# Kernel optimization log

Measured on AMD Instinct MI355X. Metric: run time of the kernel, lower is better.

The kernel has to match this reference:

```python
import jax, jax.numpy as jnp
import numpy as np

B, NB, H, C = 32, 1024, 768, 64


def setup_inputs() -> dict:
    key = jax.random.key(0)
    k1, k2, k3, k4, k5, k6 = jax.random.split(key, 6)
    block_tokens = jax.random.normal(k1, (B, NB, H), dtype=jnp.float32)
    block_active = jax.random.randint(k2, (B, NB), 0, 2) == 1
    block_to_channel_map = jax.random.randint(k3, (NB,), 0, C, dtype=jnp.int64)
    # agg_gate params: Linear(H, H//2) -> Tanh -> Linear(H//2, 1)
    s1 = 1.0 / np.sqrt(H)
    s2 = 1.0 / np.sqrt(H // 2)
    W1 = jax.random.uniform(k4, (H, H // 2), jnp.float32, -s1, s1)
    b1 = jnp.zeros((H // 2,), jnp.float32)
    W2 = jax.random.uniform(k5, (H // 2, 1), jnp.float32, -s2, s2)
    b2 = jnp.zeros((1,), jnp.float32)
    return {"block_tokens": block_tokens, "block_active": block_active,
            "block_to_channel_map": block_to_channel_map,
            "W1": W1, "b1": b1, "W2": W2, "b2": b2}


def reference(block_tokens, block_active, block_to_channel_map, W1, b1, W2, b2):
    # gate MLP: (B, NB)
    h = jnp.tanh(jnp.einsum('bnh,hk->bnk', block_tokens, W1) + b1)
    gate = (jnp.einsum('bnk,ko->bno', h, W2) + b2).squeeze(-1)  # (B, NB)

    # (C, NB) one-hot channel membership; (B, C, NB) active-per-channel mask
    onehot = block_to_channel_map[None, :] == jnp.arange(C)[:, None]
    mask = block_active[:, None, :] & onehot[None, :, :]  # (B, C, NB)

    neg_inf = jnp.float32(-jnp.inf)
    g = jnp.where(mask, gate[:, None, :], neg_inf)  # (B, C, NB)
    m = jnp.max(g, axis=-1, keepdims=True)
    m_safe = jnp.where(jnp.isfinite(m), m, 0.0)  # guard all-masked channels
    e = jnp.where(mask, jnp.exp(g - m_safe), 0.0)
    s = jnp.sum(e, axis=-1, keepdims=True)
    w = jnp.where(s > 0, e / jnp.where(s > 0, s, 1.0), 0.0)  # softmax, nan->0

    channel_tokens = jnp.einsum('bcn,bnh->bch', w, block_tokens)  # (B, C, H)
    channel_active = jnp.any(mask, axis=-1)  # (B, C)
    return channel_tokens, channel_active
```

## Files before the change

### kernel.cpp

```cpp
#include <hip/hip_runtime.h>
#include <math.h>

#define B_    32
#define NB_   1024
#define H_    768
#define K_    384
#define C_    64
#define ROWS_ 128
#define NSTEP_ 24

typedef __attribute__((ext_vector_type(8))) short bf16x8;
typedef __attribute__((ext_vector_type(4))) float f32x4;

__device__ __forceinline__ short f2bf(float f) {
    unsigned u = __float_as_uint(f);
    unsigned r = (u + 0x7fffu + ((u >> 16) & 1u)) >> 16;
    return (short)r;
}
__device__ __forceinline__ float ftanh(float x) {
    float e = __expf(2.f * x);
    return 1.f - 2.f * __builtin_amdgcn_rcpf(e + 1.f);
}

__global__ __launch_bounds__(256) void prep_w1(const float* __restrict__ W1,
                                               short* __restrict__ swz)
{
    int idx = blockIdx.x * 256 + threadIdx.x;
    int k = idx / K_, n = idx % K_;
    float v = W1[idx];
    int s = k >> 5, g = (k >> 3) & 3, i = k & 7;
    int t = n >> 4, nn = n & 15;
    swz[((s * 24 + t) * 512) + (g * 16 + nn) * 8 + i] = f2bf(v);
}

__global__ __launch_bounds__(1024) void compact_kernel(
    const int* __restrict__ active, int* __restrict__ list, int* __restrict__ cnt)
{
    __shared__ int wsum[16];
    __shared__ int wbase[17];
    const int b = blockIdx.x, tid = threadIdx.x, lane = tid & 63, wid = tid >> 6;
    const int flag = active[b * NB_ + tid] != 0;
    const unsigned long long m = __ballot(flag);
    if (lane == 0) wsum[wid] = __popcll(m);
    __syncthreads();
    if (tid == 0) {
        int r = 0;
        for (int i = 0; i < 16; ++i) { wbase[i] = r; r += wsum[i]; }
        wbase[16] = r;
        cnt[b] = r;
    }
    __syncthreads();
    const int total = wbase[16];
    if (flag) {
        const int pos = wbase[wid] + __popcll(m & ((1ull << lane) - 1ull));
        list[b * NB_ + pos] = tid;
    }
    if (tid >= total) list[b * NB_ + tid] = 0;
}

__global__ __launch_bounds__(512) void gate_kernel(
    const float* __restrict__ tokens, const short* __restrict__ swz,
    const float* __restrict__ b1, const float* __restrict__ W2,
    const float* __restrict__ b2, const int* __restrict__ list,
    const int* __restrict__ cnt, float* __restrict__ gate)
{
    __shared__ __align__(16) short As[2][4096];
    __shared__ float red[8][128];

    const int b = blockIdx.x >> 3;
    const int chunk = blockIdx.x & 7;
    if (chunk * ROWS_ >= cnt[b]) return;

    const int tid = threadIdx.x;
    const int lane = tid & 63;
    const int w = tid >> 6;

    const int arow = tid >> 2;
    const int akc  = tid & 3;
    const int nrow = list[b * NB_ + chunk * ROWS_ + arow];
    const float* aptr = tokens + ((size_t)b * NB_ + nrow) * H_ + akc * 8;

    const int aoff = (arow >> 4) * 512 + (((akc * 16 + (arow & 15)) ^ (akc * 2)) * 8);
    const int roff = (lane ^ ((lane >> 4) * 2)) * 8;
    const short* bbase = swz + (w * 3) * 512 + lane * 8;

    f32x4 acc[3][8];
#pragma unroll
    for (int j = 0; j < 3; ++j)
#pragma unroll
        for (int f = 0; f < 8; ++f) acc[j][f] = (f32x4){0.f, 0.f, 0.f, 0.f};

    float4 pe0 = *(const float4*)(aptr);
    float4 pe1 = *(const float4*)(aptr + 4);
    float4 po0 = *(const float4*)(aptr + 32);
    float4 po1 = *(const float4*)(aptr + 36);
    bf16x8 be0 = *(const bf16x8*)(bbase);
    bf16x8 be1 = *(const bf16x8*)(bbase + 512);
    bf16x8 be2 = *(const bf16x8*)(bbase + 1024);
    bf16x8 bo0 = be0, bo1 = be1, bo2 = be2;
    {
        bf16x8 av = {f2bf(pe0.x), f2bf(pe0.y), f2bf(pe0.z), f2bf(pe0.w),
                     f2bf(pe1.x), f2bf(pe1.y), f2bf(pe1.z), f2bf(pe1.w)};
        *(bf16x8*)&As[0][aoff] = av;
    }
    asm volatile("s_waitcnt lgkmcnt(0)" ::: "memory");
    __builtin_amdgcn_s_barrier();
    __builtin_amdgcn_sched_barrier(0);

#define GATE_ITER(S, PA0, PA1, QA0, QA1, BC0, BC1, BC2, BN0, BN1, BN2)        \
    do {                                                                      \
        if ((S) + 2 < NSTEP_) {                                               \
            PA0 = *(const float4*)(aptr + ((S) + 2) * 32);                    \
            PA1 = *(const float4*)(aptr + ((S) + 2) * 32 + 4);                \
        }                                                                     \
        if ((S) + 1 < NSTEP_) {                                               \
            const short* bp = bbase + ((S) + 1) * 12288;                      \
            BN0 = *(const bf16x8*)(bp);                                       \
            BN1 = *(const bf16x8*)(bp + 512);                                 \
            BN2 = *(const bf16x8*)(bp + 1024);                                \
            bf16x8 av = {f2bf(QA0.x), f2bf(QA0.y), f2bf(QA0.z), f2bf(QA0.w),  \
                         f2bf(QA1.x), f2bf(QA1.y), f2bf(QA1.z), f2bf(QA1.w)}; \
            *(bf16x8*)&As[((S) + 1) & 1][aoff] = av;                          \
        }                                                                     \
        _Pragma("unroll")                                                     \
        for (int f = 0; f < 8; ++f) {                                         \
            bf16x8 af = *(const bf16x8*)&As[(S) & 1][f * 512 + roff];         \
            acc[0][f] = __builtin_amdgcn_mfma_f32_16x16x32_bf16(af, BC0, acc[0][f], 0, 0, 0); \
            acc[1][f] = __builtin_amdgcn_mfma_f32_16x16x32_bf16(af, BC1, acc[1][f], 0, 0, 0); \
            acc[2][f] = __builtin_amdgcn_mfma_f32_16x16x32_bf16(af, BC2, acc[2][f], 0, 0, 0); \
        }                                                                     \
        asm volatile("s_waitcnt lgkmcnt(0)" ::: "memory");                    \
        __builtin_amdgcn_s_barrier();                                         \
        __builtin_amdgcn_sched_barrier(0);                                    \
    } while (0)

    for (int s = 0; s < NSTEP_; s += 2) {
        GATE_ITER(s,     pe0, pe1, po0, po1, be0, be1, be2, bo0, bo1, bo2);
        GATE_ITER(s + 1, po0, po1, pe0, pe1, bo0, bo1, bo2, be0, be1, be2);
    }
#undef GATE_ITER

    float ps[8][4];
#pragma unroll
    for (int f = 0; f < 8; ++f)
#pragma unroll
        for (int r = 0; r < 4; ++r) ps[f][r] = 0.f;

#pragma unroll
    for (int j = 0; j < 3; ++j) {
        const int n = (w * 3 + j) * 16 + (lane & 15);
        const float bb = b1[n];
        const float ww = W2[n];
#pragma unroll
        for (int f = 0; f < 8; ++f)
#pragma unroll
            for (int r = 0; r < 4; ++r)
                ps[f][r] += ftanh(acc[j][f][r] + bb) * ww;
    }
#pragma unroll
    for (int m = 1; m < 16; m <<= 1)
#pragma unroll
        for (int f = 0; f < 8; ++f)
#pragma unroll
            for (int r = 0; r < 4; ++r)
                ps[f][r] += __shfl_xor(ps[f][r], m, 64);

    if ((lane & 15) == 0) {
        const int rbase = (lane >> 4) * 4;
#pragma unroll
        for (int f = 0; f < 8; ++f)
#pragma unroll
            for (int r = 0; r < 4; ++r)
                red[w][f * 16 + rbase + r] = ps[f][r];
    }
    __syncthreads();
    if (tid < ROWS_) {
        float sg = b2[0];
#pragma unroll
        for (int q = 0; q < 8; ++q) sg += red[q][tid];
        gate[b * NB_ + list[b * NB_ + chunk * ROWS_ + tid]] = sg;
    }
}

__global__ __launch_bounds__(256) void agg_kernel(
    const float* __restrict__ tokens, const int* __restrict__ active,
    const int* __restrict__ cmap, const float* __restrict__ gate,
    float* __restrict__ out_tok, float* __restrict__ out_act)
{
    __shared__ float wls[NB_];
    __shared__ float red[256];
    __shared__ int   idxs[NB_];
    __shared__ float wts[NB_];
    __shared__ int   gbase[17];

    const int b = blockIdx.x >> 6, c = blockIdx.x & 63;
    const int tid = threadIdx.x, lane = tid & 63, wid = tid >> 6;

    float lmax = -INFINITY;
    for (int n = tid; n < NB_; n += 256) {
        const bool msk = (active[b * NB_ + n] != 0) && (cmap[n] == c);
        const float g  = msk ? gate[b * NB_ + n] : -INFINITY;
        wls[n] = g;
        lmax = fmaxf(lmax, g);
    }
    red[tid] = lmax; __syncthreads();
    for (int s = 128; s > 0; s >>= 1) {
        if (tid < s) red[tid] = fmaxf(red[tid], red[tid + s]);
        __syncthreads();
    }
    const float m = red[0]; __syncthreads();
    const float msafe = (m > -INFINITY) ? m : 0.f;

    float lsum = 0.f;
    for (int n = tid; n < NB_; n += 256) {
        const float g = wls[n];
        const float e = (g > -INFINITY) ? __expf(g - msafe) : 0.f;
        wls[n] = e; lsum += e;
    }
    red[tid] = lsum; __syncthreads();
    for (int s = 128; s > 0; s >>= 1) {
        if (tid < s) red[tid] += red[tid + s];
        __syncthreads();
    }
    const float ssum = red[0];
    const float inv  = (ssum > 0.f) ? 1.f / ssum : 0.f;
    __syncthreads();

#pragma unroll
    for (int it = 0; it < 4; ++it) {
        const int n = it * 256 + wid * 64 + lane;
        const unsigned long long mask = __ballot(wls[n] > 0.f);
        if (lane == 0) gbase[1 + it * 4 + wid] = __popcll(mask);
    }
    __syncthreads();
    if (tid == 0) {
        gbase[0] = 0;
        for (int i = 1; i <= 16; ++i) gbase[i] += gbase[i - 1];
    }
    __syncthreads();
#pragma unroll
    for (int it = 0; it < 4; ++it) {
        const int n = it * 256 + wid * 64 + lane;
        const float e = wls[n];
        const unsigned long long mask = __ballot(e > 0.f);
        if (e > 0.f) {
            const int pos = gbase[it * 4 + wid] +
                            __popcll(mask & ((1ull << lane) - 1ull));
            idxs[pos] = n;
            wts[pos]  = e * inv;
        }
    }
    __syncthreads();
    const int cnt = gbase[16];

    float a0 = 0.f, a1 = 0.f, a2 = 0.f;
    const float* tb = tokens + (size_t)b * NB_ * H_;
    for (int i = 0; i < cnt; ++i) {
        const float wv = wts[i];
        const float* t = tb + (size_t)idxs[i] * H_;
        a0 += wv * t[tid];
        a1 += wv * t[tid + 256];
        a2 += wv * t[tid + 512];
    }
    float* o = out_tok + ((size_t)(b * C_ + c)) * H_;
    o[tid]       = a0;
    o[tid + 256] = a1;
    o[tid + 512] = a2;
    if (tid == 0) out_act[b * C_ + c] = (m > -INFINITY) ? 1.f : 0.f;
}

extern "C" void kernel_launch(void* const* d_in, const int* in_sizes, int n_in,
                              void* d_out, int out_size, void* d_ws, size_t ws_size,
                              hipStream_t stream)
{
    const float* tokens = (const float*)d_in[0];
    const int*   active = (const int*)  d_in[1];
    const int*   cmap   = (const int*)  d_in[2];
    const float* W1     = (const float*)d_in[3];
    const float* b1     = (const float*)d_in[4];
    const float* W2     = (const float*)d_in[5];
    const float* b2     = (const float*)d_in[6];

    float* out      = (float*)d_out;
    float* out_act  = out + (size_t)B_ * C_ * H_;

    short* swz     = (short*)d_ws;
    float* gate_ws = (float*)((char*)d_ws + 589824);
    int*   list    = (int*)  ((char*)d_ws + 720896);
    int*   cntb    = (int*)  ((char*)d_ws + 851968);

    compact_kernel<<<B_, 1024, 0, stream>>>(active, list, cntb);
    prep_w1<<<(H_ * K_) / 256, 256, 0, stream>>>(W1, swz);
    gate_kernel<<<B_ * 8, 512, 0, stream>>>(tokens, swz, b1, W2, b2, list, cntb, gate_ws);
    agg_kernel<<<B_ * C_, 256, 0, stream>>>(tokens, active, cmap, gate_ws, out, out_act);
}
```

Before: 55.94 us.

## Shrink gate tiles to 32 rows with 256-thread blocks; vectorize agg loads

The gate GEMM now uses 32-row tiles and 256-thread blocks, giving 1024 blocks instead of 256. Each wave covers 6 N-tiles over 2 row fragments, and occupancy is hinted at 3 blocks per SM. This spreads the active rows over more CUs, at the cost of reloading the W1 slices once per block, which means more global traffic for B. The aggregation kernel switches to float4 loads using 192 threads, cutting the instruction count but leaving a quarter of the threads idle.

```diff
diff --git a/kernel.cpp b/kernel.cpp
--- a/kernel.cpp
+++ b/kernel.cpp
@@ -6,7 +6,7 @@
 #define H_    768
 #define K_    384
 #define C_    64
-#define ROWS_ 128
+#define ROWS_ 32
 #define NSTEP_ 24
 
 typedef __attribute__((ext_vector_type(8))) short bf16x8;
@@ -58,126 +58,158 @@
     if (tid >= total) list[b * NB_ + tid] = 0;
 }
 
-__global__ __launch_bounds__(512) void gate_kernel(
+__global__ __launch_bounds__(256, 3) void gate_kernel(
     const float* __restrict__ tokens, const short* __restrict__ swz,
     const float* __restrict__ b1, const float* __restrict__ W2,
     const float* __restrict__ b2, const int* __restrict__ list,
     const int* __restrict__ cnt, float* __restrict__ gate)
 {
-    __shared__ __align__(16) short As[2][4096];
-    __shared__ float red[8][128];
-
-    const int b = blockIdx.x >> 3;
-    const int chunk = blockIdx.x & 7;
+    __shared__ __align__(16) short As[2][1024];
+    __shared__ float red[4][32];
+
+    const int b = blockIdx.x >> 5;
+    const int chunk = blockIdx.x & 31;
     if (chunk * ROWS_ >= cnt[b]) return;
 
     const int tid = threadIdx.x;
     const int lane = tid & 63;
     const int w = tid >> 6;
 
-    const int arow = tid >> 2;
-    const int akc  = tid & 3;
-    const int nrow = list[b * NB_ + chunk * ROWS_ + arow];
-    const float* aptr = tokens + ((size_t)b * NB_ + nrow) * H_ + akc * 8;
-
-    const int aoff = (arow >> 4) * 512 + (((akc * 16 + (arow & 15)) ^ (akc * 2)) * 8);
-    const int roff = (lane ^ ((lane >> 4) * 2)) * 8;
-    const short* bbase = swz + (w * 3) * 512 + lane * 8;
-
-    f32x4 acc[3][8];
-#pragma unroll
-    for (int j = 0; j < 3; ++j)
-#pragma unroll
-        for (int f = 0; f < 8; ++f) acc[j][f] = (f32x4){0.f, 0.f, 0.f, 0.f};
-
-    float4 pe0 = *(const float4*)(aptr);
-    float4 pe1 = *(const float4*)(aptr + 4);
-    float4 po0 = *(const float4*)(aptr + 32);
-    float4 po1 = *(const float4*)(aptr + 36);
+    const int r   = tid >> 3;
+    const int c8  = tid & 7;
+    const int g2w = c8 >> 1, hw = c8 & 1;
+    const int fw  = r >> 4,  roww = r & 15;
+    const int woff = ((fw * 4 + g2w) * 16 + (roww ^ (g2w << 1))) * 8 + hw * 4;
+    const int nrow = list[b * NB_ + chunk * ROWS_ + r];
+    const float* aptr = tokens + ((size_t)b * NB_ + nrow) * H_ + c8 * 4;
+
+    const int g2r  = lane >> 4;
+    const int rowr = (lane & 15) ^ (g2r << 1);
+    const int roff0 = ((0 + g2r) * 16 + rowr) * 8;
+    const int roff1 = ((4 + g2r) * 16 + rowr) * 8;
+
+    const short* bbase = swz + (w * 6) * 512 + lane * 8;
+
+    f32x4 acc[6][2];
+#pragma unroll
+    for (int j = 0; j < 6; ++j)
+#pragma unroll
+        for (int f = 0; f < 2; ++f) acc[j][f] = (f32x4){0.f, 0.f, 0.f, 0.f};
+
+    float4 pe = *(const float4*)(aptr);
+    float4 po = *(const float4*)(aptr + 32);
     bf16x8 be0 = *(const bf16x8*)(bbase);
     bf16x8 be1 = *(const bf16x8*)(bbase + 512);
     bf16x8 be2 = *(const bf16x8*)(bbase + 1024);
-    bf16x8 bo0 = be0, bo1 = be1, bo2 = be2;
+    bf16x8 be3 = *(const bf16x8*)(bbase + 1536);
+    bf16x8 be4 = *(const bf16x8*)(bbase + 2048);
+    bf16x8 be5 = *(const bf16x8*)(bbase + 2560);
+    bf16x8 bo0 = be0, bo1 = be1, bo2 = be2, bo3 = be3, bo4 = be4, bo5 = be5;
     {
-        bf16x8 av = {f2bf(pe0.x), f2bf(pe0.y), f2bf(pe0.z), f2bf(pe0.w),
-                     f2bf(pe1.x), f2bf(pe1.y), f2bf(pe1.z), f2bf(pe1.w)};
-        *(bf16x8*)&As[0][aoff] = av;
+        short4 av = {f2bf(pe.x), f2bf(pe.y), f2bf(pe.z), f2bf(pe.w)};
+        *(short4*)&As[0][woff] = av;
     }
     asm volatile("s_waitcnt lgkmcnt(0)" ::: "memory");
     __builtin_amdgcn_s_barrier();
     __builtin_amdgcn_sched_barrier(0);
 
-#define GATE_ITER(S, PA0, PA1, QA0, QA1, BC0, BC1, BC2, BN0, BN1, BN2)        \
+#define MFMA_STEP(BUF, B0, B1, B2, B3, B4, B5)                                \
     do {                                                                      \
-        if ((S) + 2 < NSTEP_) {                                               \
-            PA0 = *(const float4*)(aptr + ((S) + 2) * 32);                    \
-            PA1 = *(const float4*)(aptr + ((S) + 2) * 32 + 4);                \
-        }                                                                     \
-        if ((S) + 1 < NSTEP_) {                                               \
-            const short* bp = bbase + ((S) + 1) * 12288;                      \
-            BN0 = *(const bf16x8*)(bp);                                       \
-            BN1 = *(const bf16x8*)(bp + 512);                                 \
-            BN2 = *(const bf16x8*)(bp + 1024);                                \
-            bf16x8 av = {f2bf(QA0.x), f2bf(QA0.y), f2bf(QA0.z), f2bf(QA0.w),  \
-                         f2bf(QA1.x), f2bf(QA1.y), f2bf(QA1.z), f2bf(QA1.w)}; \
-            *(bf16x8*)&As[((S) + 1) & 1][aoff] = av;                          \
-        }                                                                     \
-        _Pragma("unroll")                                                     \
-        for (int f = 0; f < 8; ++f) {                                         \
-            bf16x8 af = *(const bf16x8*)&As[(S) & 1][f * 512 + roff];         \
-            acc[0][f] = __builtin_amdgcn_mfma_f32_16x16x32_bf16(af, BC0, acc[0][f], 0, 0, 0); \
-            acc[1][f] = __builtin_amdgcn_mfma_f32_16x16x32_bf16(af, BC1, acc[1][f], 0, 0, 0); \
-            acc[2][f] = __builtin_amdgcn_mfma_f32_16x16x32_bf16(af, BC2, acc[2][f], 0, 0, 0); \
-        }                                                                     \
-        asm volatile("s_waitcnt lgkmcnt(0)" ::: "memory");                    \
-        __builtin_amdgcn_s_barrier();                                         \
-        __builtin_amdgcn_sched_barrier(0);                                    \
+        bf16x8 a0 = *(const bf16x8*)&As[BUF][roff0];                          \
+        bf16x8 a1 = *(const bf16x8*)&As[BUF][roff1];                          \
+        acc[0][0] = __builtin_amdgcn_mfma_f32_16x16x32_bf16(a0, B0, acc[0][0], 0, 0, 0); \
+        acc[0][1] = __builtin_amdgcn_mfma_f32_16x16x32_bf16(a1, B0, acc[0][1], 0, 0, 0); \
+        acc[1][0] = __builtin_amdgcn_mfma_f32_16x16x32_bf16(a0, B1, acc[1][0], 0, 0, 0); \
+        acc[1][1] = __builtin_amdgcn_mfma_f32_16x16x32_bf16(a1, B1, acc[1][1], 0, 0, 0); \
+        acc[2][0] = __builtin_amdgcn_mfma_f32_16x16x32_bf16(a0, B2, acc[2][0], 0, 0, 0); \
+        acc[2][1] = __builtin_amdgcn_mfma_f32_16x16x32_bf16(a1, B2, acc[2][1], 0, 0, 0); \
+        acc[3][0] = __builtin_amdgcn_mfma_f32_16x16x32_bf16(a0, B3, acc[3][0], 0, 0, 0); \
+        acc[3][1] = __builtin_amdgcn_mfma_f32_16x16x32_bf16(a1, B3, acc[3][1], 0, 0, 0); \
+        acc[4][0] = __builtin_amdgcn_mfma_f32_16x16x32_bf16(a0, B4, acc[4][0], 0, 0, 0); \
+        acc[4][1] = __builtin_amdgcn_mfma_f32_16x16x32_bf16(a1, B4, acc[4][1], 0, 0, 0); \
+        acc[5][0] = __builtin_amdgcn_mfma_f32_16x16x32_bf16(a0, B5, acc[5][0], 0, 0, 0); \
+        acc[5][1] = __builtin_amdgcn_mfma_f32_16x16x32_bf16(a1, B5, acc[5][1], 0, 0, 0); \
     } while (0)
 
     for (int s = 0; s < NSTEP_; s += 2) {
-        GATE_ITER(s,     pe0, pe1, po0, po1, be0, be1, be2, bo0, bo1, bo2);
-        GATE_ITER(s + 1, po0, po1, pe0, pe1, bo0, bo1, bo2, be0, be1, be2);
-    }
-#undef GATE_ITER
-
-    float ps[8][4];
-#pragma unroll
-    for (int f = 0; f < 8; ++f)
-#pragma unroll
-        for (int r = 0; r < 4; ++r) ps[f][r] = 0.f;
-
-#pragma unroll
-    for (int j = 0; j < 3; ++j) {
-        const int n = (w * 3 + j) * 16 + (lane & 15);
+        if (s + 2 < NSTEP_) pe = *(const float4*)(aptr + (s + 2) * 32);
+        if (s + 1 < NSTEP_) {
+            const short* bp = bbase + (s + 1) * 12288;
+            bo0 = *(const bf16x8*)(bp);
+            bo1 = *(const bf16x8*)(bp + 512);
+            bo2 = *(const bf16x8*)(bp + 1024);
+            bo3 = *(const bf16x8*)(bp + 1536);
+            bo4 = *(const bf16x8*)(bp + 2048);
+            bo5 = *(const bf16x8*)(bp + 2560);
+        }
+        MFMA_STEP(0, be0, be1, be2, be3, be4, be5);
+        if (s + 1 < NSTEP_) {
+            short4 av = {f2bf(po.x), f2bf(po.y), f2bf(po.z), f2bf(po.w)};
+            *(short4*)&As[1][woff] = av;
+        }
+        asm volatile("s_waitcnt lgkmcnt(0)" ::: "memory");
+        __builtin_amdgcn_s_barrier();
+        __builtin_amdgcn_sched_barrier(0);
+
+        if (s + 3 < NSTEP_) po = *(const float4*)(aptr + (s + 3) * 32);
+        if (s + 2 < NSTEP_) {
+            const short* bp = bbase + (s + 2) * 12288;
+            be0 = *(const bf16x8*)(bp);
+            be1 = *(const bf16x8*)(bp + 512);
+            be2 = *(const bf16x8*)(bp + 1024);
+            be3 = *(const bf16x8*)(bp + 1536);
+            be4 = *(const bf16x8*)(bp + 2048);
+            be5 = *(const bf16x8*)(bp + 2560);
+        }
+        MFMA_STEP(1, bo0, bo1, bo2, bo3, bo4, bo5);
+        if (s + 2 < NSTEP_) {
+            short4 av = {f2bf(pe.x), f2bf(pe.y), f2bf(pe.z), f2bf(pe.w)};
+            *(short4*)&As[0][woff] = av;
+        }
+        asm volatile("s_waitcnt lgkmcnt(0)" ::: "memory");
+        __builtin_amdgcn_s_barrier();
+        __builtin_amdgcn_sched_barrier(0);
+    }
+#undef MFMA_STEP
+
+    float ps[2][4];
+#pragma unroll
+    for (int f = 0; f < 2; ++f)
+#pragma unroll
+        for (int rr = 0; rr < 4; ++rr) ps[f][rr] = 0.f;
+
+#pragma unroll
+    for (int j = 0; j < 6; ++j) {
+        const int n = (w * 6 + j) * 16 + (lane & 15);
         const float bb = b1[n];
         const float ww = W2[n];
 #pragma unroll
-        for (int f = 0; f < 8; ++f)
-#pragma unroll
-            for (int r = 0; r < 4; ++r)
-                ps[f][r] += ftanh(acc[j][f][r] + bb) * ww;
+        for (int f = 0; f < 2; ++f)
+#pragma unroll
+            for (int rr = 0; rr < 4; ++rr)
+                ps[f][rr] += ftanh(acc[j][f][rr] + bb) * ww;
     }
 #pragma unroll
     for (int m = 1; m < 16; m <<= 1)
 #pragma unroll
-        for (int f = 0; f < 8; ++f)
-#pragma unroll
-            for (int r = 0; r < 4; ++r)
-                ps[f][r] += __shfl_xor(ps[f][r], m, 64);
+        for (int f = 0; f < 2; ++f)
+#pragma unroll
+            for (int rr = 0; rr < 4; ++rr)
+                ps[f][rr] += __shfl_xor(ps[f][rr], m, 64);
 
     if ((lane & 15) == 0) {
         const int rbase = (lane >> 4) * 4;
 #pragma unroll
-        for (int f = 0; f < 8; ++f)
-#pragma unroll
-            for (int r = 0; r < 4; ++r)
-                red[w][f * 16 + rbase + r] = ps[f][r];
+        for (int f = 0; f < 2; ++f)
+#pragma unroll
+            for (int rr = 0; rr < 4; ++rr)
+                red[w][f * 16 + rbase + rr] = ps[f][rr];
     }
     __syncthreads();
     if (tid < ROWS_) {
         float sg = b2[0];
 #pragma unroll
-        for (int q = 0; q < 8; ++q) sg += red[q][tid];
+        for (int q = 0; q < 4; ++q) sg += red[q][tid];
         gate[b * NB_ + list[b * NB_ + chunk * ROWS_ + tid]] = sg;
     }
 }
@@ -253,19 +285,18 @@
     __syncthreads();
     const int cnt = gbase[16];
 
-    float a0 = 0.f, a1 = 0.f, a2 = 0.f;
-    const float* tb = tokens + (size_t)b * NB_ * H_;
-    for (int i = 0; i < cnt; ++i) {
-        const float wv = wts[i];
-        const float* t = tb + (size_t)idxs[i] * H_;
-        a0 += wv * t[tid];
-        a1 += wv * t[tid + 256];
-        a2 += wv * t[tid + 512];
-    }
-    float* o = out_tok + ((size_t)(b * C_ + c)) * H_;
-    o[tid]       = a0;
-    o[tid + 256] = a1;
-    o[tid + 512] = a2;
+    if (tid < 192) {
+        const int d = tid * 4;
+        const float* tb = tokens + (size_t)b * NB_ * H_ + d;
+        float4 a = {0.f, 0.f, 0.f, 0.f};
+        for (int i = 0; i < cnt; ++i) {
+            const float wv = wts[i];
+            const float4 v = *(const float4*)(tb + (size_t)idxs[i] * H_);
+            a.x += wv * v.x; a.y += wv * v.y;
+            a.z += wv * v.z; a.w += wv * v.w;
+        }
+        *(float4*)(out_tok + ((size_t)(b * C_ + c)) * H_ + d) = a;
+    }
     if (tid == 0) out_act[b * C_ + c] = (m > -INFINITY) ? 1.f : 0.f;
 }
 
@@ -291,6 +322,6 @@
 
     compact_kernel<<<B_, 1024, 0, stream>>>(active, list, cntb);
     prep_w1<<<(H_ * K_) / 256, 256, 0, stream>>>(W1, swz);
-    gate_kernel<<<B_ * 8, 512, 0, stream>>>(tokens, swz, b1, W2, b2, list, cntb, gate_ws);
+    gate_kernel<<<B_ * 32, 256, 0, stream>>>(tokens, swz, b1, W2, b2, list, cntb, gate_ws);
     agg_kernel<<<B_ * C_, 256, 0, stream>>>(tokens, active, cmap, gate_ws, out, out_act);
 }
```

Result: slower. 60.16 us (+7.5%).
